# Kernel tuning notes

Hardware: AMD Instinct MI355X
Metric: run time of the kernel (lower is better)

## Reference

```python
import jax, jax.numpy as jnp
import numpy as np
import math

B, CIN, H, W = 8, 64, 128, 128
IC = 128           # inter_channel
CMIN = 32
FN = 3             # feature_num
PLANES = CMIN * 2  # BNL planes
GROUPS = 8
ORDER = 2
GAMMA = 1e-4
FEAT_SHAPES = [(64, 128, 128), (128, 64, 64), (256, 32, 32)]

_pm_cache = {}

def _pool_mat(n, s):
    # adaptive avg-pool matrix [s, n] (torch AdaptiveAvgPool2d bin rule)
    key = (n, s)
    if key not in _pm_cache:
        m = np.zeros((s, n), np.float32)
        for j in range(s):
            a = (j * n) // s
            b = -((-(j + 1) * n) // s)
            m[j, a:b] = 1.0 / (b - a)
        _pm_cache[key] = jnp.asarray(m)
    return _pm_cache[key]

def _pap(x):
    # pyramidAP: adaptive avg pool to 1,3,6,8 and flatten -> [b,c,110]
    b, c, hh, ww = x.shape
    outs = []
    for s in (1, 3, 6, 8):
        ph, pw = _pool_mat(hh, s), _pool_mat(ww, s)
        outs.append(jnp.einsum('ph,bchw,qw->bcpq', ph, x, pw).reshape(b, c, s * s))
    return jnp.concatenate(outs, axis=2)

def _c1x1(w, x):
    return jnp.einsum('oi,bihw->bohw', w, x)

def _pad1(x):
    # kernel_size=1, padding=1 conv == 1x1 conv then zero-pad spatially by 1
    return jnp.pad(x, ((0, 0), (0, 0), (1, 1), (1, 1)))

def _conv3(w, x):
    return jax.lax.conv_general_dilated(x, w, (1, 1), 'SAME',
                                        dimension_numbers=('NCHW', 'OIHW', 'NCHW'))

def _bnl(x_high, x_low, t_w, p_w, g_w, z_w, gn_w, gn_b):
    b, c, h, w = x_high.shape
    # per-group flattened 'single token' vectors of length (planes/G)*h*w
    t = _c1x1(t_w, x_high).reshape(b, GROUPS, -1)
    p = _c1x1(p_w, x_low).reshape(b, GROUPS, -1)
    g = _c1x1(g_w, x_low).reshape(b, GROUPS, -1)
    alphas = [math.sqrt((2 * GAMMA) ** k / math.factorial(k) * math.exp(-2 * GAMMA))
              for k in range(ORDER + 1)]
    t_tay = jnp.stack([t ** k * alphas[k] for k in range(ORDER + 1)], axis=2)  # [b,G,3,N]
    p_tay = jnp.stack([p ** k * alphas[k] for k in range(ORDER + 1)], axis=2)
    att = jnp.einsum('bgkn,bgn->bgk', p_tay, g)          # [b,G,3]
    x = jnp.einsum('bgk,bgkn->bgn', att, t_tay).reshape(b, PLANES, h, w)
    # grouped 1x1 conv z (groups=8)
    x = jnp.einsum('goi,bgihw->bgohw', z_w,
                   x.reshape(b, GROUPS, PLANES // GROUPS, h, w)).reshape(b, c, h, w)
    # GroupNorm(8, 64)
    xg = x.reshape(b, GROUPS, -1)
    mu = xg.mean(-1, keepdims=True)
    var = xg.var(-1, keepdims=True)
    xn = ((xg - mu) / jnp.sqrt(var + 1e-5)).reshape(b, c, h, w)
    xn = xn * gn_w[None, :, None, None] + gn_b[None, :, None, None]
    return xn + x_high

def setup_inputs() -> dict:
    key = jax.random.key(0)
    ks = iter(jax.random.split(key, 64))
    def rn(shape, scale=1.0):
        return jax.random.normal(next(ks), shape, jnp.float32) * scale
    inp = {'input_g': rn((B, CIN, H, W)), 'input_c': rn((B, CIN, H, W))}
    for i, (c, hh, ww) in enumerate(FEAT_SHAPES):
        inp[f'fg_{i}'] = rn((B, c, hh, ww))
        inp[f'fc_{i}'] = rn((B, c, hh, ww))
        for nm in ('k1', 'v1', 'k2', 'v2'):
            inp[f'{nm}_w_{i}'] = rn((IC, c), 0.05)
    inp['q1_w'] = rn((IC, CIN, 3, 3), 0.05)
    inp['q2_w'] = rn((IC, CIN, 3, 3), 0.05)
    inp['mask1_w'] = rn((CIN, IC + CIN), 0.05)
    inp['mask2_w'] = rn((CIN, IC + CIN), 0.05)
    inp['fuse1_w'] = rn((CIN, CIN * FN), 0.05)
    inp['fuse2_w'] = rn((CIN, CIN * FN), 0.05)
    inp['t_w'] = rn((PLANES, CIN), 0.05)
    inp['p_w'] = rn((PLANES, CIN), 0.05)
    inp['g_w'] = rn((PLANES, CIN), 0.05)
    inp['z_w'] = rn((GROUPS, CIN // GROUPS, PLANES // GROUPS), 0.05)
    inp['gn_w'] = jnp.ones((CIN,), jnp.float32)
    inp['gn_b'] = jnp.zeros((CIN,), jnp.float32)
    return inp

def reference(input_g, input_c, fg_0, fg_1, fg_2, fc_0, fc_1, fc_2,
              q1_w, q2_w,
              k1_w_0, v1_w_0, k2_w_0, v2_w_0,
              k1_w_1, v1_w_1, k2_w_1, v2_w_1,
              k1_w_2, v1_w_2, k2_w_2, v2_w_2,
              mask1_w, mask2_w, fuse1_w, fuse2_w,
              t_w, p_w, g_w, z_w, gn_w, gn_b):
    b, c, h, w = input_g.shape
    n = h * w
    x_q1 = _conv3(q1_w, input_g).reshape(b, IC, n)
    x_q2 = _conv3(q2_w, input_c).reshape(b, IC, n)
    fgs = [fg_0, fg_1, fg_2]
    fcs = [fc_0, fc_1, fc_2]
    k1s = [k1_w_0, k1_w_1, k1_w_2]
    v1s = [v1_w_0, v1_w_1, v1_w_2]
    k2s = [k2_w_0, k2_w_1, k2_w_2]
    v2s = [v2_w_0, v2_w_1, v2_w_2]
    grays, colors = [], []
    for i in range(FN):
        xk1 = _pap(_pad1(_c1x1(k1s[i], fcs[i])))   # [b,IC,110]
        xk2 = _pap(_pad1(_c1x1(k2s[i], fgs[i])))
        xv1 = _pap(_pad1(_c1x1(v1s[i], fcs[i])))
        xv2 = _pap(_pad1(_c1x1(v2s[i], fgs[i])))
        kq1 = jax.nn.softmax(jnp.clip(jnp.einsum('bcp,bcn->bpn', xk1, x_q1), -64, 64), axis=1)
        kq2 = jax.nn.softmax(jnp.clip(jnp.einsum('bcp,bcn->bpn', xk2, x_q2), -64, 64), axis=1)
        vkq1 = jnp.einsum('bcp,bpn->bcn', xv1, kq1).reshape(b, IC, h, w)
        vkq2 = jnp.einsum('bcp,bpn->bcn', xv2, kq2).reshape(b, IC, h, w)
        grays.append(_c1x1(mask1_w, jnp.concatenate([input_g, vkq1], 1)))
        colors.append(_c1x1(mask2_w, jnp.concatenate([input_c, vkq2], 1)))
    x_gray = jnp.tanh(_c1x1(fuse1_w, jnp.concatenate(grays, 1))) + input_g
    x_color = jnp.tanh(_c1x1(fuse2_w, jnp.concatenate(colors, 1))) + input_c
    return _bnl(x_gray, x_color, t_w, p_w, g_w, z_w, gn_w, gn_b) + input_g
```

## Files before the change

### kernel.cpp

```cpp
#include <hip/hip_runtime.h>
#include <math.h>

constexpr int    BB      = 8;
constexpr int    NN      = 16384;
constexpr size_t SZ_XQ_ST = (size_t)BB * 128 * NN;
constexpr size_t SZ_XF_ST = (size_t)BB * 64 * NN;

constexpr size_t OFF_XQ   = 0;
constexpr size_t OFF_XT   = 16777216;
constexpr size_t OFF_XF   = 33554432;
constexpr size_t OFF_XG   = OFF_XF + 8388608;
constexpr size_t OFF_POOL = OFF_XF + 2 * SZ_XF_ST;
constexpr size_t OFF_XK   = OFF_POOL + 788480;
constexpr size_t OFF_XV   = OFF_XK + 344064;
constexpr size_t OFF_MT   = OFF_XV + 688128;
constexpr size_t OFF_W    = OFF_MT + 393216;
constexpr size_t OFF_AT   = OFF_W + 73728;
constexpr size_t OFF_WT   = OFF_AT + 4096;
constexpr size_t OFF_ATTC = OFF_WT + 12288;
constexpr size_t OFF_MV   = OFF_ATTC + 192;
constexpr size_t OFF_PART = OFF_MV + 128;
constexpr size_t OFF_PART2= OFF_PART + 98304;

#define A0SQ 0.9998000199986667f
#define A1SQ 1.9996000399973335e-4f
#define A2SQ 1.9996000399973334e-8f

typedef __attribute__((ext_vector_type(8))) short bf16x8;
typedef __attribute__((ext_vector_type(4))) float f32x4;

__device__ inline ushort f2bf(float f) {
    uint u = __float_as_uint(f);
    return (ushort)((u + 0x7fffu + ((u >> 16) & 1u)) >> 16);
}
__device__ inline float bf2f(ushort u) { return __uint_as_float((uint)u << 16); }
__device__ inline uint pk2bf(float lo, float hi) {
    return (uint)f2bf(lo) | ((uint)f2bf(hi) << 16);
}

__global__ __launch_bounds__(256) void k_xt(const float* __restrict__ in0, const float* __restrict__ in1,
                                            ushort* __restrict__ xt0, ushort* __restrict__ xt1) {
    __shared__ float L[64 * 130];
    const int y = blockIdx.x, b = blockIdx.y, tid = threadIdx.x;
    const float* in = blockIdx.z ? in1 : in0;
    ushort* xt = blockIdx.z ? xt1 : xt0;
    const float* ib = in + (((size_t)b * 64) << 14) + (y << 7);
    for (int r = 0; r < 32; ++r) {
        int idx = tid + (r << 8); int ch = idx >> 7; int x = idx & 127;
        L[ch * 130 + x] = ib[((size_t)ch << 14) + x];
    }
    __syncthreads();
    const int x = tid >> 1, seg = tid & 1;
    ushort* ob = xt + ((size_t)(b * 128 + y) * 128 + x) * 64 + seg * 32;
    uint pk[16];
#pragma unroll
    for (int c = 0; c < 16; ++c)
        pk[c] = pk2bf(L[(seg * 32 + 2 * c) * 130 + x], L[(seg * 32 + 2 * c + 1) * 130 + x]);
    uint4* o4 = (uint4*)ob;
#pragma unroll
    for (int c = 0; c < 4; ++c) o4[c] = make_uint4(pk[4 * c], pk[4 * c + 1], pk[4 * c + 2], pk[4 * c + 3]);
}

__global__ __launch_bounds__(256) void k_wt(const float* __restrict__ w1, const float* __restrict__ w2,
                                            ushort* __restrict__ wt1, ushort* __restrict__ wt2) {
    int id = blockIdx.x * 256 + threadIdx.x;
    if (id >= 147456) return;
    int cs = id / 73728; int rem = id - cs * 73728;
    int t = rem >> 13; int oc = (rem >> 6) & 127; int ic = rem & 63;
    const float* w = cs ? w2 : w1;
    (cs ? wt2 : wt1)[rem] = f2bf(w[((size_t)(oc * 64 + ic)) * 9 + t]);
}

__global__ __launch_bounds__(256, 2) void k_convm2(const ushort* __restrict__ Xt0, const ushort* __restrict__ Xt1,
                                                   const ushort* __restrict__ Wt0, const ushort* __restrict__ Wt1,
                                                   ushort* __restrict__ out_base) {
    __shared__ ushort smem[3 * 130 * 72];
    const int tid = threadIdx.x;
    const int y = blockIdx.x, b = blockIdx.y;
    const ushort* Xt = blockIdx.z ? Xt1 : Xt0;
    const ushort* Wt = blockIdx.z ? Wt1 : Wt0;
    ushort* out = out_base + (size_t)blockIdx.z * 16777216;
    const int l = tid & 63;
    const int wv = __builtin_amdgcn_readfirstlane(tid >> 6);
    const int lr = l & 15;
    const int q = l >> 4;

    for (int slot = tid; slot < 390; slot += 256) {
        int dy = slot / 130, xx = slot - dy * 130;
        int row = y + dy - 1, sx = xx - 1;
        bool v = (row >= 0) & (row < 128) & (sx >= 0) & (sx < 128);
        const uint4* s = (const uint4*)(Xt + (((size_t)(b * 128 + row) * 128 + sx) * 64));
        uint4* d = (uint4*)(smem + (size_t)slot * 72);
        uint4 z = make_uint4(0, 0, 0, 0);
#pragma unroll
        for (int j = 0; j < 8; ++j) d[j] = v ? s[j] : z;
    }
    __syncthreads();

    f32x4 acc[2][8];
#pragma unroll
    for (int f = 0; f < 2; ++f)
#pragma unroll
        for (int g = 0; g < 8; ++g)
// ... 7 lines not shown
        for (int h = 0; h < 2; ++h) {
            const int ko = h * 32 + q * 8;
            bf16x8 a0 = *(const bf16x8*)(Wt + ((size_t)(t * 128 + wv * 32 + lr) * 64 + ko));
            bf16x8 a1 = *(const bf16x8*)(Wt + ((size_t)(t * 128 + wv * 32 + 16 + lr) * 64 + ko));
#pragma unroll
            for (int g = 0; g < 8; ++g) {
                bf16x8 bb = *(const bf16x8*)(smem + (size_t)(dy * 130 + g * 16 + lr + dx) * 72 + ko);
                acc[0][g] = __builtin_amdgcn_mfma_f32_16x16x32_bf16(a0, bb, acc[0][g], 0, 0, 0);
                acc[1][g] = __builtin_amdgcn_mfma_f32_16x16x32_bf16(a1, bb, acc[1][g], 0, 0, 0);
            }
        }
    }
    __syncthreads();
    uint* T = (uint*)smem;
#pragma unroll
    for (int f = 0; f < 2; ++f)
#pragma unroll
        for (int g = 0; g < 8; ++g) {
            int dw = (g * 16 + lr) * 68 + wv * 16 + f * 8 + q * 2;
            T[dw] = pk2bf(acc[f][g][0], acc[f][g][1]);
            T[dw + 1] = pk2bf(acc[f][g][2], acc[f][g][3]);
        }
    __syncthreads();
    const int x = tid >> 1, sg = tid & 1;
    ushort* ob = out + ((size_t)(b * 128 + y) * 128 + x) * 128 + sg * 64;
    const uint* src = &T[x * 68 + sg * 32];
#pragma unroll
    for (int j = 0; j < 8; ++j) {
        uint4 vv = *(const uint4*)(src + 4 * j);
        *(uint4*)(ob + j * 8) = vv;
    }
}

struct PoolPtrs { const float* src[6]; };

__global__ __launch_bounds__(256) void k_pool2(PoolPtrs pp, float* __restrict__ ws) {
    extern __shared__ float P[];
    const int blk = blockIdx.x;
    const int tid = threadIdx.x;
    if (blk < 1024) {
        const int tI = (blk < 512) ? 0 : 3;
        const int local = (blk < 512) ? blk : blk - 512;
        const size_t toff = (tI == 0) ? 0 : 394240;
        const int h = 128, stride = 129;
        const float* img = pp.src[tI] + (size_t)local * h * h;
        for (int f = tid; f < h * h; f += 256) {
            int r = f >> 7; int cc = f & 127;
            P[r * stride + cc] = img[f];
        }
        __syncthreads();
        if (tid < h) {
            float cur = 0.f; const int rb = tid * stride;
            for (int cc = 0; cc < h; ++cc) { cur += P[rb + cc]; P[rb + cc] = cur; }
        }
        __syncthreads();
        if (tid < h) {
            float cur = 0.f;
            for (int r = 0; r < h; ++r) { int a = r * stride + tid; cur += P[a]; P[a] = cur; }
        }
        __syncthreads();
        if (tid < 110) {
            int s, off2;
            if (tid == 0)      { s = 1; off2 = 0; }
            else if (tid < 10) { s = 3; off2 = 1; }
            else if (tid < 46) { s = 6; off2 = 10; }
            else               { s = 8; off2 = 46; }
            int r = tid - off2; int j = r / s; int q = r - j * s;
            const int n = h + 2;
            int ra = (j * n) / s,       rb2 = ((j + 1) * n + s - 1) / s;
            int ca = (q * n) / s,       cb2 = ((q + 1) * n + s - 1) / s;
            float area = (float)((rb2 - ra) * (cb2 - ca));
            int r0 = ra - 1; if (r0 < 0) r0 = 0;  int r1 = rb2 - 1; if (r1 > h) r1 = h;
            int c0 = ca - 1; if (c0 < 0) c0 = 0;  int c1 = cb2 - 1; if (c1 > h) c1 = h;
            float ssum = 0.f;
            if (r1 > r0 && c1 > c0) {
                int ri = r1 - 1, rj = r0 - 1, ci = c1 - 1, cj = c0 - 1;
                float f11 = P[ri * stride + ci];
                float f01 = (rj < 0) ? 0.f : P[rj * stride + ci];
                float f10 = (cj < 0) ? 0.f : P[ri * stride + cj];
                float f00 = (rj < 0 || cj < 0) ? 0.f : P[rj * stride + cj];
                ssum = f11 - f01 - f10 + f00;
            }
            ws[OFF_POOL + toff + (size_t)local * 110 + tid] = ssum / area;
        }
    } else {
        int h, hs, tI, local0;
        if (blk < 1536) {
            h = 64; hs = 6;
            if (blk < 1280) { tI = 1; local0 = (blk - 1024) * 4; }
            else            { tI = 4; local0 = (blk - 1280) * 4; }
        } else {
            h = 32; hs = 5;
            if (blk < 1792) { tI = 2; local0 = (blk - 1536) * 8; }
            else            { tI = 5; local0 = (blk - 1792) * 8; }
        }
        const size_t toff = (tI == 1) ? 56320 : (tI == 4) ? 450560 : (tI == 2) ? 168960 : 563200;
        const int lg = tid >> hs;
        const int lr = tid & (h - 1);
        const int stride = h + 1;
        float* Pb = P + (size_t)lg * h * stride;
        const float* img = pp.src[tI] + (size_t)(local0 + lg) * h * h;
        for (int f = lr; f < h * h; f += h) {
            int r = f >> hs; int cc = f & (h - 1);
            Pb[r * stride + cc] = img[f];
        }
        __syncthreads();
        {
            float cur = 0.f; const int rb = lr * stride;
            for (int cc = 0; cc < h; ++cc) { cur += Pb[rb + cc]; Pb[rb + cc] = cur; }
        }
        __syncthreads();
        {
            float cur = 0.f;
            for (int r = 0; r < h; ++r) { int a = r * stride + lr; cur += Pb[a]; Pb[a] = cur; }
        }
        __syncthreads();
        for (int t = lr; t < 110; t += h) {
            int s, off2;
            if (t == 0)      { s = 1; off2 = 0; }
            else if (t < 10) { s = 3; off2 = 1; }
            else if (t < 46) { s = 6; off2 = 10; }
            else             { s = 8; off2 = 46; }
            int r = t - off2; int j = r / s; int q = r - j * s;
            const int n = h + 2;
            int ra = (j * n) / s,       rb2 = ((j + 1) * n + s - 1) / s;
            int ca = (q * n) / s,       cb2 = ((q + 1) * n + s - 1) / s;
            float area = (float)((rb2 - ra) * (cb2 - ca));
            int r0 = ra - 1; if (r0 < 0) r0 = 0;  int r1 = rb2 - 1; if (r1 > h) r1 = h;
            int c0 = ca - 1; if (c0 < 0) c0 = 0;  int c1 = cb2 - 1; if (c1 > h) c1 = h;
            float ssum = 0.f;
            if (r1 > r0 && c1 > c0) {
                int ri = r1 - 1, rj = r0 - 1, ci = c1 - 1, cj = c0 - 1;
                float f11 = Pb[ri * stride + ci];
                float f01 = (rj < 0) ? 0.f : Pb[rj * stride + ci];
                float f10 = (cj < 0) ? 0.f : Pb[ri * stride + cj];
                float f00 = (rj < 0 || cj < 0) ? 0.f : Pb[rj * stride + cj];
                ssum = f11 - f01 - f10 + f00;
            }
            ws[OFF_POOL + toff + (size_t)(local0 + lg) * 110 + t] = ssum / area;
        }
    }
}

__global__ __launch_bounds__(256) void k_pkw(const float* __restrict__ f1, const float* __restrict__ f2,
                                             const float* __restrict__ m1, const float* __restrict__ m2,
                                             const float* __restrict__ tw, const float* __restrict__ pw,
                                             const float* __restrict__ gw, float* __restrict__ ws) {
    int id = blockIdx.x * 256 + threadIdx.x;
    if (id < 73728) {
        int c = id % 192; int t = id / 192; int o = t & 63; int t2 = t >> 6; int i = t2 % 3; int st = t2 / 3;
        const float* fu = st ? f2 : f1; const float* ma = st ? m2 : m1;
        float s = 0.f;
        for (int k = 0; k < 64; ++k) s = fmaf(fu[o * 192 + i * 64 + k], ma[k * 192 + c], s);
        ws[OFF_W + id] = s;
    } else if (id < 81920) {
        int x = id - 73728; int o = x & 63; int c = (x >> 6) & 63; int st = x >> 12;
        const float* fu = st ? f2 : f1; const float* ma = st ? m2 : m1;
        float s = 0.f;
        for (int k = 0; k < 192; ++k) s = fmaf(fu[o * 192 + k], ma[(k & 63) * 192 + c], s);
        ((ushort*)(ws + OFF_AT))[(size_t)st * 4096 + o * 64 + c] = f2bf(s);
    } else if (id < 94208) {
        int x = id - 81920; int c = x & 63; int o = (x >> 6) & 63; int f = x >> 12;
        const float* src = (f == 0) ? tw : ((f == 1) ? pw : gw);
        ((ushort*)(ws + OFF_WT))[(size_t)f * 4096 + o * 64 + c] = f2bf(src[o * 64 + c]);
    }
}

struct KvPtrs { const float* k1[3]; const float* k2[3]; const float* v1[3]; const float* v2[3]; };

__global__ __launch_bounds__(256) void k_xkxv(KvPtrs kp, float* __restrict__ ws) {
    int id = blockIdx.x * 256 + threadIdx.x;
    int isV = 0;
    if (id >= 688128) { isV = 1; id -= 688128; }
    int p = id % 112; int t1 = id / 112; int C = t1 & 127; int t2 = t1 >> 7;
    int b = t2 & 7; int t3 = t2 >> 3; int i = t3 % 3; int st = t3 / 3;
    const int ci = 64 << i;
    size_t poff = (size_t)st * 394240 + (i >= 1 ? 56320 : 0) + (i >= 2 ? 112640 : 0);
    const float* kw = isV ? (st ? kp.v2[i] : kp.v1[i]) : (st ? kp.k2[i] : kp.k1[i]);
    float s = 0.f;
    if (p < 110) {
        const float* pl = ws + OFF_POOL + poff + (size_t)b * ci * 110 + p;
        for (int ic = 0; ic < ci; ++ic) s = fmaf(kw[C * ci + ic], pl[(size_t)ic * 110], s);
    }
    if (isV) ws[OFF_XV + id] = s;
    else     ((ushort*)(ws + OFF_XK))[(size_t)t2 * 14336 + p * 128 + C] = f2bf(s);
}

__global__ __launch_bounds__(256) void k_mt(float* __restrict__ ws) {
    int id = blockIdx.x * 256 + threadIdx.x;
    int p = id & 127; int o = (id >> 7) & 63; int t2 = id >> 13;
    int sti = t2 >> 3;
    float s = 0.f;
    if (p < 110) {
        const float* Wrow = ws + OFF_W + ((size_t)sti * 64 + o) * 192 + 64;
        const float* xv = ws + OFF_XV + (size_t)t2 * 128 * 112 + p;
        for (int r = 0; r < 128; ++r) s = fmaf(Wrow[r], xv[(size_t)r * 112], s);
    }
    ((ushort*)(ws + OFF_MT))[id] = f2bf(s);
}

__global__ __launch_bounds__(256, 2) void k_attn7(float* __restrict__ ws,
                                                  const float* __restrict__ g_in,
                                                  const float* __restrict__ c_in) {
    __shared__ uint pbuf[128 * 68];
    const int tid = threadIdx.x;
    const int w = __builtin_amdgcn_readfirstlane(tid >> 6);
    const int l = tid & 63;
    const int lr = l & 15;
    const int g4 = l >> 4;
    const int n0 = blockIdx.x << 7;
    const int b = blockIdx.y;
    const int st = blockIdx.z;

    const ushort* xqb = (const ushort*)(ws + OFF_XQ);
    const ushort* xkb = (const ushort*)(ws + OFF_XK);
    const ushort* mtb = (const ushort*)(ws + OFF_MT);
    const ushort* atb = (const ushort*)(ws + OFF_AT) + (size_t)st * 4096;
    const ushort* xt  = (const ushort*)(ws + OFF_XT) + (size_t)st * 8388608 + ((size_t)b << 14) * 64;

    {
        int row = w * 32 + (l >> 1);
        int dcol = 56 + ((l & 1) << 2);
#pragma unroll
        for (int j = 0; j < 4; ++j) pbuf[row * 68 + dcol + j] = 0;
    }
    const int ng0 = n0 + (2 * w + 0) * 16 + lr;
    const int ng1 = n0 + (2 * w + 1) * 16 + lr;
    const int row0 = w * 32 + lr;
    const int row1 = w * 32 + 16 + lr;
// ... 206 lines not shown
                    bf16x8 a_p = *(const bf16x8*)(wtb + 4096 + ao);
                    bf16x8 a_g = *(const bf16x8*)(wtb + 8192 + ao);
                    ap_[m] = __builtin_amdgcn_mfma_f32_16x16x32_bf16(a_p, bx, ap_[m], 0, 0, 0);
                    ag_[m] = __builtin_amdgcn_mfma_f32_16x16x32_bf16(a_g, bx, ag_[m], 0, 0, 0);
                }
            }
#pragma unroll
            for (int m = 0; m < 4; ++m)
#pragma unroll
                for (int r = 0; r < 4; ++r) {
                    float pv = ap_[m][r], gv = ag_[m][r];
                    s[m][0] += gv;
                    s[m][1] = fmaf(pv, gv, s[m][1]);
                    s[m][2] = fmaf(pv * pv, gv, s[m][2]);
                }
        }
#pragma unroll
        for (int off = 1; off < 32; off <<= 1)
#pragma unroll
            for (int m = 0; m < 4; ++m)
#pragma unroll
                for (int k = 0; k < 3; ++k) s[m][k] += __shfl_xor(s[m][k], off);
        if (l == 0 || l == 32) {
            const int h = g4 >> 1;
#pragma unroll
            for (int m = 0; m < 4; ++m)
#pragma unroll
                for (int k = 0; k < 3; ++k)
                    ws[OFF_PART + (size_t)((b * 8 + 2 * m + h) * 3 + k) * 512 + blockIdx.x * 4 + w] = s[m][k];
        }
    }
}

__global__ __launch_bounds__(64) void k_attc(float* __restrict__ ws) {
    const int id = blockIdx.x;
    const int l = threadIdx.x;
    const float4* v = (const float4*)(ws + OFF_PART + (size_t)id * 512 + l * 8);
    float4 a = v[0], b2 = v[1];
    float s = a.x + a.y + a.z + a.w + b2.x + b2.y + b2.z + b2.w;
#pragma unroll
    for (int off = 1; off < 64; off <<= 1) s += __shfl_xor(s, off);
    if (l == 0) ws[OFF_ATTC + id] = s;
}

__global__ __launch_bounds__(256) void k_stats2(float* __restrict__ ws, const float* __restrict__ zw) {
    __shared__ float r0[256], r1[256];
    const int nc = blockIdx.x, g = blockIdx.y, b = blockIdx.z, tid = threadIdx.x;
    const ushort* tfb = (const ushort*)(ws + OFF_XF) + ((size_t)(b * 64 + g * 8) << 14);
    const float* a = ws + OFF_ATTC + (size_t)(b * 8 + g) * 3;
    const float c0 = A0SQ * a[0], c1 = A1SQ * a[1], c2 = A2SQ * a[2];
    const float* z = zw + (size_t)g * 64;
    float sum = 0.f, ssq = 0.f;
    for (int n = nc * 2048 + tid; n < (nc + 1) * 2048; n += 256) {
        float y[8];
#pragma unroll
        for (int pl = 0; pl < 8; ++pl) { float tv = bf2f(tfb[((size_t)pl << 14) + n]); y[pl] = fmaf(fmaf(c2, tv, c1), tv, c0); }
#pragma unroll
        for (int o = 0; o < 8; ++o) {
            float xz = 0.f;
#pragma unroll
            for (int i2 = 0; i2 < 8; ++i2) xz = fmaf(z[o * 8 + i2], y[i2], xz);
            sum += xz; ssq = fmaf(xz, xz, ssq);
        }
    }
    r0[tid] = sum; r1[tid] = ssq;
    __syncthreads();
    for (int w = 128; w > 0; w >>= 1) {
        if (tid < w) { r0[tid] += r0[tid + w]; r1[tid] += r1[tid + w]; }
        __syncthreads();
    }
    if (tid == 0) {
        float* p2 = ws + OFF_PART2 + (size_t)((b * 8 + g) * 8 + nc) * 2;
        p2[0] = r0[0]; p2[1] = r1[0];
    }
}

__global__ __launch_bounds__(64) void k_mv(float* __restrict__ ws) {
    const int t = threadIdx.x;
    float sum = 0.f, ssq = 0.f;
    const float* p2 = ws + OFF_PART2 + (size_t)t * 16;
#pragma unroll
    for (int nc = 0; nc < 8; ++nc) { sum += p2[nc * 2]; ssq += p2[nc * 2 + 1]; }
    float mean = sum * (1.f / 131072.f);
    float var = ssq * (1.f / 131072.f) - mean * mean;
    float* mv = ws + OFF_MV + (size_t)t * 2;
    mv[0] = mean; mv[1] = rsqrtf(var + 1e-5f);
}

__global__ __launch_bounds__(256) void k_final(float* __restrict__ ws, const float* __restrict__ zw,
                                               const float* __restrict__ gnw, const float* __restrict__ gnb,
                                               const float* __restrict__ g_in, float* __restrict__ out) {
    int id = blockIdx.x * 256 + threadIdx.x;
    int n = id & 16383; int g = (id >> 14) & 7; int b = id >> 17;
    const float* a = ws + OFF_ATTC + (size_t)(b * 8 + g) * 3;
    const float c0 = A0SQ * a[0], c1 = A1SQ * a[1], c2 = A2SQ * a[2];
    const float* mv = ws + OFF_MV + (size_t)(b * 8 + g) * 2;
    const float mean = mv[0], istd = mv[1];
    const float* z = zw + (size_t)g * 64;
    const ushort* tfb = (const ushort*)(ws + OFF_XF) + ((size_t)(b * 64 + g * 8) << 14) + n;
    float y[8];
#pragma unroll
    for (int pl = 0; pl < 8; ++pl) { float tv = bf2f(tfb[(size_t)pl << 14]); y[pl] = fmaf(fmaf(c2, tv, c1), tv, c0); }
    const ushort* thb = (const ushort*)(ws + OFF_XG) + (((size_t)b << 14) + n) * 64 + g * 8;
    ushort4 u0 = *(const ushort4*)thb;
    ushort4 u1 = *(const ushort4*)(thb + 4);
    float thv[8] = { bf2f(u0.x), bf2f(u0.y), bf2f(u0.z), bf2f(u0.w),
                     bf2f(u1.x), bf2f(u1.y), bf2f(u1.z), bf2f(u1.w) };
    const size_t cb = ((size_t)(b * 64 + g * 8) << 14) + n;
    const float* gi = g_in + cb;
    float* op = out + cb;
#pragma unroll
    for (int o = 0; o < 8; ++o) {
        float xz = 0.f;
#pragma unroll
        for (int i2 = 0; i2 < 8; ++i2) xz = fmaf(z[o * 8 + i2], y[i2], xz);
        int ch = g * 8 + o;
        float base = fmaf((xz - mean) * istd, gnw[ch], gnb[ch]) + thv[o];
        op[(size_t)o << 14] = fmaf(2.f, gi[(size_t)o << 14], base);
    }
}

extern "C" void kernel_launch(void* const* d_in, const int* in_sizes, int n_in,
                              void* d_out, int out_size, void* d_ws, size_t ws_size,
                              hipStream_t stream) {
    const float* in_g = (const float*)d_in[0];
    const float* in_c = (const float*)d_in[1];
    float* ws = (float*)d_ws;
    float* out = (float*)d_out;

    ushort* xqb  = (ushort*)(ws + OFF_XQ);
    ushort* xt_g = (ushort*)(ws + OFF_XT);
    ushort* xt_c = xt_g + 8388608;
    ushort* wt_g = (ushort*)(ws + OFF_XF);
    ushort* wt_c = wt_g + 73728;

    k_xt<<<dim3(128, 8, 2), 256, 0, stream>>>(in_g, in_c, xt_g, xt_c);
    k_wt<<<576, 256, 0, stream>>>((const float*)d_in[20], (const float*)d_in[21], wt_g, wt_c);

    k_convm2<<<dim3(128, 8, 2), 256, 0, stream>>>(xt_g, xt_c, wt_g, wt_c, xqb);

    PoolPtrs pp;
    pp.src[0] = (const float*)d_in[3];  pp.src[1] = (const float*)d_in[9];  pp.src[2] = (const float*)d_in[15];
    pp.src[3] = (const float*)d_in[2];  pp.src[4] = (const float*)d_in[8];  pp.src[5] = (const float*)d_in[14];
    k_pool2<<<2048, 256, 66560, stream>>>(pp, ws);

    k_pkw<<<368, 256, 0, stream>>>((const float*)d_in[24], (const float*)d_in[25],
                                   (const float*)d_in[22], (const float*)d_in[23],
                                   (const float*)d_in[26], (const float*)d_in[27],
                                   (const float*)d_in[28], ws);

    KvPtrs kp;
    kp.k1[0] = (const float*)d_in[4];  kp.k1[1] = (const float*)d_in[10]; kp.k1[2] = (const float*)d_in[16];
    kp.k2[0] = (const float*)d_in[6];  kp.k2[1] = (const float*)d_in[12]; kp.k2[2] = (const float*)d_in[18];
    kp.v1[0] = (const float*)d_in[5];  kp.v1[1] = (const float*)d_in[11]; kp.v1[2] = (const float*)d_in[17];
    kp.v2[0] = (const float*)d_in[7];  kp.v2[1] = (const float*)d_in[13]; kp.v2[2] = (const float*)d_in[19];
    k_xkxv<<<5376, 256, 0, stream>>>(kp, ws);

    k_mt<<<3072, 256, 0, stream>>>(ws);

    k_attn7<<<dim3(128, 8, 2), 256, 0, stream>>>(ws, in_g, in_c);

    k_attc<<<192, 64, 0, stream>>>(ws);

    k_stats2<<<dim3(8, 8, 8), 256, 0, stream>>>(ws, (const float*)d_in[29]);
    k_mv<<<1, 64, 0, stream>>>(ws);
    k_final<<<4096, 256, 0, stream>>>(ws, (const float*)d_in[29], (const float*)d_in[30],
                                      (const float*)d_in[31], in_g, out);
}
```

Baseline: 540.6 us.

## Merge prep kernels, reassociate value-weight product, and fold tiny reductions into neighbors

Folds the transpose, weight conversion, weight-packing and pyramid pooling kernels into one launch. It also reassociates the value path so the fused mask weight is multiplied into the value conv weights first (a small weight-only product) instead of into pooled features per batch. The attention-coefficient and mean/variance reduction kernels are absorbed into the stats and final kernels. The goal is to cut launch count and some per-batch FLOPs. The cost is redundant small reductions per block and a heavier, heterogeneous prep kernel with large shared memory applied to all its blocks.

```diff
diff --git a/kernel.cpp b/kernel.cpp
--- a/kernel.cpp
+++ b/kernel.cpp
@@ -38,37 +38,170 @@
     return (uint)f2bf(lo) | ((uint)f2bf(hi) << 16);
 }
 
-__global__ __launch_bounds__(256) void k_xt(const float* __restrict__ in0, const float* __restrict__ in1,
-                                            ushort* __restrict__ xt0, ushort* __restrict__ xt1) {
-    __shared__ float L[64 * 130];
-    const int y = blockIdx.x, b = blockIdx.y, tid = threadIdx.x;
-    const float* in = blockIdx.z ? in1 : in0;
-    ushort* xt = blockIdx.z ? xt1 : xt0;
-    const float* ib = in + (((size_t)b * 64) << 14) + (y << 7);
-    for (int r = 0; r < 32; ++r) {
-        int idx = tid + (r << 8); int ch = idx >> 7; int x = idx & 127;
-        L[ch * 130 + x] = ib[((size_t)ch << 14) + x];
-    }
-    __syncthreads();
-    const int x = tid >> 1, seg = tid & 1;
-    ushort* ob = xt + ((size_t)(b * 128 + y) * 128 + x) * 64 + seg * 32;
-    uint pk[16];
-#pragma unroll
-    for (int c = 0; c < 16; ++c)
-        pk[c] = pk2bf(L[(seg * 32 + 2 * c) * 130 + x], L[(seg * 32 + 2 * c + 1) * 130 + x]);
-    uint4* o4 = (uint4*)ob;
-#pragma unroll
-    for (int c = 0; c < 4; ++c) o4[c] = make_uint4(pk[4 * c], pk[4 * c + 1], pk[4 * c + 2], pk[4 * c + 3]);
-}
-
-__global__ __launch_bounds__(256) void k_wt(const float* __restrict__ w1, const float* __restrict__ w2,
-                                            ushort* __restrict__ wt1, ushort* __restrict__ wt2) {
-    int id = blockIdx.x * 256 + threadIdx.x;
-    if (id >= 147456) return;
-    int cs = id / 73728; int rem = id - cs * 73728;
-    int t = rem >> 13; int oc = (rem >> 6) & 127; int ic = rem & 63;
-    const float* w = cs ? w2 : w1;
-    (cs ? wt2 : wt1)[rem] = f2bf(w[((size_t)(oc * 64 + ic)) * 9 + t]);
+struct PrepPtrs {
+    const float* in_g; const float* in_c;
+    const float* w1;  const float* w2;
+    const float* f1;  const float* f2; const float* m1; const float* m2;
+    const float* tw;  const float* pw; const float* gw;
+    const float* pool[6];
+};
+
+__global__ __launch_bounds__(256) void k_prep(PrepPtrs pp, float* __restrict__ ws) {
+    extern __shared__ float P[];
+    const int blk = blockIdx.x;
+    const int tid = threadIdx.x;
+    if (blk < 2048) {
+        const int z = blk >> 10, b = (blk >> 7) & 7, y = blk & 127;
+        const float* in = z ? pp.in_c : pp.in_g;
+        ushort* xt = (ushort*)(ws + OFF_XT) + (size_t)z * 8388608;
+        float* L = P;
+        const float* ib = in + (((size_t)b * 64) << 14) + (y << 7);
+        for (int r = 0; r < 32; ++r) {
+            int idx = tid + (r << 8); int ch = idx >> 7; int x = idx & 127;
+            L[ch * 130 + x] = ib[((size_t)ch << 14) + x];
+        }
+        __syncthreads();
+        const int x = tid >> 1, seg = tid & 1;
+        ushort* ob = xt + ((size_t)(b * 128 + y) * 128 + x) * 64 + seg * 32;
+        uint pk[16];
+#pragma unroll
+        for (int c = 0; c < 16; ++c)
+            pk[c] = pk2bf(L[(seg * 32 + 2 * c) * 130 + x], L[(seg * 32 + 2 * c + 1) * 130 + x]);
+        uint4* o4 = (uint4*)ob;
+#pragma unroll
+        for (int c = 0; c < 4; ++c) o4[c] = make_uint4(pk[4 * c], pk[4 * c + 1], pk[4 * c + 2], pk[4 * c + 3]);
+    } else if (blk < 2624) {
+        int id = (blk - 2048) * 256 + tid;
+        if (id >= 147456) return;
+        int cs = id / 73728; int rem = id - cs * 73728;
+        int t = rem >> 13; int oc = (rem >> 6) & 127; int ic = rem & 63;
+        const float* w = cs ? pp.w2 : pp.w1;
+        ushort* wt = (ushort*)(ws + OFF_XF) + (size_t)cs * 73728;
+        wt[rem] = f2bf(w[((size_t)(oc * 64 + ic)) * 9 + t]);
+    } else if (blk < 2992) {
+        int id = (blk - 2624) * 256 + tid;
+        if (id < 73728) {
+            int c = id % 192; int t = id / 192; int o = t & 63; int t2 = t >> 6; int i = t2 % 3; int st = t2 / 3;
+            const float* fu = st ? pp.f2 : pp.f1; const float* ma = st ? pp.m2 : pp.m1;
+            float s = 0.f;
+            for (int k = 0; k < 64; ++k) s = fmaf(fu[o * 192 + i * 64 + k], ma[k * 192 + c], s);
+            ws[OFF_W + id] = s;
+        } else if (id < 81920) {
+            int x = id - 73728; int o = x & 63; int c = (x >> 6) & 63; int st = x >> 12;
+            const float* fu = st ? pp.f2 : pp.f1; const float* ma = st ? pp.m2 : pp.m1;
+            float s = 0.f;
+            for (int k = 0; k < 192; ++k) s = fmaf(fu[o * 192 + k], ma[(k & 63) * 192 + c], s);
+            ((ushort*)(ws + OFF_AT))[(size_t)st * 4096 + o * 64 + c] = f2bf(s);
+        } else if (id < 94208) {
+            int x = id - 81920; int c = x & 63; int o = (x >> 6) & 63; int f = x >> 12;
+            const float* src = (f == 0) ? pp.tw : ((f == 1) ? pp.pw : pp.gw);
+            ((ushort*)(ws + OFF_WT))[(size_t)f * 4096 + o * 64 + c] = f2bf(src[o * 64 + c]);
+        }
+    } else {
+        const int pblk = blk - 2992;
+        if (pblk < 1024) {
+            const int tI = (pblk < 512) ? 0 : 3;
+            const int local = (pblk < 512) ? pblk : pblk - 512;
+            const size_t toff = (tI == 0) ? 0 : 394240;
+            const int h = 128, stride = 129;
+            const float* img = pp.pool[tI] + (size_t)local * h * h;
+            for (int f = tid; f < h * h; f += 256) {
+                int r = f >> 7; int cc = f & 127;
+                P[r * stride + cc] = img[f];
+            }
+            __syncthreads();
+            if (tid < h) {
+                float cur = 0.f; const int rb = tid * stride;
+                for (int cc = 0; cc < h; ++cc) { cur += P[rb + cc]; P[rb + cc] = cur; }
+            }
+            __syncthreads();
+            if (tid < h) {
+                float cur = 0.f;
+                for (int r = 0; r < h; ++r) { int a = r * stride + tid; cur += P[a]; P[a] = cur; }
+            }
+            __syncthreads();
+            if (tid < 110) {
+                int s, off2;
+                if (tid == 0)      { s = 1; off2 = 0; }
+                else if (tid < 10) { s = 3; off2 = 1; }
+                else if (tid < 46) { s = 6; off2 = 10; }
+                else               { s = 8; off2 = 46; }
+                int r = tid - off2; int j = r / s; int q = r - j * s;
+                const int n = h + 2;
+                int ra = (j * n) / s,       rb2 = ((j + 1) * n + s - 1) / s;
+                int ca = (q * n) / s,       cb2 = ((q + 1) * n + s - 1) / s;
+                float area = (float)((rb2 - ra) * (cb2 - ca));
+                int r0 = ra - 1; if (r0 < 0) r0 = 0;  int r1 = rb2 - 1; if (r1 > h) r1 = h;
+                int c0 = ca - 1; if (c0 < 0) c0 = 0;  int c1 = cb2 - 1; if (c1 > h) c1 = h;
+                float ssum = 0.f;
+                if (r1 > r0 && c1 > c0) {
+                    int ri = r1 - 1, rj = r0 - 1, ci = c1 - 1, cj = c0 - 1;
+                    float f11 = P[ri * stride + ci];
+                    float f01 = (rj < 0) ? 0.f : P[rj * stride + ci];
+                    float f10 = (cj < 0) ? 0.f : P[ri * stride + cj];
+                    float f00 = (rj < 0 || cj < 0) ? 0.f : P[rj * stride + cj];
+                    ssum = f11 - f01 - f10 + f00;
+                }
+                ws[OFF_POOL + toff + (size_t)local * 110 + tid] = ssum / area;
+            }
+        } else {
+            int h, hs, tI, local0;
+            if (pblk < 1536) {
+                h = 64; hs = 6;
+                if (pblk < 1280) { tI = 1; local0 = (pblk - 1024) * 4; }
+                else             { tI = 4; local0 = (pblk - 1280) * 4; }
+            } else {
+                h = 32; hs = 5;
+                if (pblk < 1792) { tI = 2; local0 = (pblk - 1536) * 8; }
+                else             { tI = 5; local0 = (pblk - 1792) * 8; }
+            }
+            const size_t toff = (tI == 1) ? 56320 : (tI == 4) ? 450560 : (tI == 2) ? 168960 : 563200;
+            const int lg = tid >> hs;
+            const int lr = tid & (h - 1);
+            const int stride = h + 1;
+            float* Pb = P + (size_t)lg * h * stride;
+            const float* img = pp.pool[tI] + (size_t)(local0 + lg) * h * h;
+            for (int f = lr; f < h * h; f += h) {
+                int r = f >> hs; int cc = f & (h - 1);
+                Pb[r * stride + cc] = img[f];
+            }
+            __syncthreads();
+            {
+                float cur = 0.f; const int rb = lr * stride;
+                for (int cc = 0; cc < h; ++cc) { cur += Pb[rb + cc]; Pb[rb + cc] = cur; }
+            }
+            __syncthreads();
+            {
+                float cur = 0.f;
+                for (int r = 0; r < h; ++r) { int a = r * stride + lr; cur += Pb[a]; Pb[a] = cur; }
+            }
+            __syncthreads();
+            for (int t = lr; t < 110; t += h) {
+                int s, off2;
+                if (t == 0)      { s = 1; off2 = 0; }
+                else if (t < 10) { s = 3; off2 = 1; }
+                else if (t < 46) { s = 6; off2 = 10; }
+                else             { s = 8; off2 = 46; }
+                int r = t - off2; int j = r / s; int q = r - j * s;
+                const int n = h + 2;
+                int ra = (j * n) / s,       rb2 = ((j + 1) * n + s - 1) / s;
+                int ca = (q * n) / s,       cb2 = ((q + 1) * n + s - 1) / s;
+                float area = (float)((rb2 - ra) * (cb2 - ca));
+                int r0 = ra - 1; if (r0 < 0) r0 = 0;  int r1 = rb2 - 1; if (r1 > h) r1 = h;
+                int c0 = ca - 1; if (c0 < 0) c0 = 0;  int c1 = cb2 - 1; if (c1 > h) c1 = h;
+                float ssum = 0.f;
+                if (r1 > r0 && c1 > c0) {
+                    int ri = r1 - 1, rj = r0 - 1, ci = c1 - 1, cj = c0 - 1;
+                    float f11 = Pb[ri * stride + ci];
+                    float f01 = (rj < 0) ? 0.f : Pb[rj * stride + ci];
+                    float f10 = (cj < 0) ? 0.f : Pb[ri * stride + cj];
+                    float f00 = (rj < 0 || cj < 0) ? 0.f : Pb[rj * stride + cj];
+                    ssum = f11 - f01 - f10 + f00;
+                }
+                ws[OFF_POOL + toff + (size_t)(local0 + lg) * 110 + t] = ssum / area;
+            }
+        }
+    }
 }
 
 __global__ __launch_bounds__(256, 2) void k_convm2(const ushort* __restrict__ Xt0, const ushort* __restrict__ Xt1,
@@ -142,169 +275,50 @@
     }
 }
 
-struct PoolPtrs { const float* src[6]; };
-
-__global__ __launch_bounds__(256) void k_pool2(PoolPtrs pp, float* __restrict__ ws) {
-    extern __shared__ float P[];
-    const int blk = blockIdx.x;
-    const int tid = threadIdx.x;
-    if (blk < 1024) {
-        const int tI = (blk < 512) ? 0 : 3;
-        const int local = (blk < 512) ? blk : blk - 512;
-        const size_t toff = (tI == 0) ? 0 : 394240;
-        const int h = 128, stride = 129;
-        const float* img = pp.src[tI] + (size_t)local * h * h;
-        for (int f = tid; f < h * h; f += 256) {
-            int r = f >> 7; int cc = f & 127;
-            P[r * stride + cc] = img[f];
-        }
-        __syncthreads();
-        if (tid < h) {
-            float cur = 0.f; const int rb = tid * stride;
-            for (int cc = 0; cc < h; ++cc) { cur += P[rb + cc]; P[rb + cc] = cur; }
-        }
-        __syncthreads();
-        if (tid < h) {
-            float cur = 0.f;
-            for (int r = 0; r < h; ++r) { int a = r * stride + tid; cur += P[a]; P[a] = cur; }
-        }
-        __syncthreads();
-        if (tid < 110) {
-            int s, off2;
-            if (tid == 0)      { s = 1; off2 = 0; }
-            else if (tid < 10) { s = 3; off2 = 1; }
-            else if (tid < 46) { s = 6; off2 = 10; }
-            else               { s = 8; off2 = 46; }
-            int r = tid - off2; int j = r / s; int q = r - j * s;
-            const int n = h + 2;
-            int ra = (j * n) / s,       rb2 = ((j + 1) * n + s - 1) / s;
-            int ca = (q * n) / s,       cb2 = ((q + 1) * n + s - 1) / s;
-            float area = (float)((rb2 - ra) * (cb2 - ca));
-            int r0 = ra - 1; if (r0 < 0) r0 = 0;  int r1 = rb2 - 1; if (r1 > h) r1 = h;
-            int c0 = ca - 1; if (c0 < 0) c0 = 0;  int c1 = cb2 - 1; if (c1 > h) c1 = h;
-            float ssum = 0.f;
-            if (r1 > r0 && c1 > c0) {
-                int ri = r1 - 1, rj = r0 - 1, ci = c1 - 1, cj = c0 - 1;
-                float f11 = P[ri * stride + ci];
-                float f01 = (rj < 0) ? 0.f : P[rj * stride + ci];
-                float f10 = (cj < 0) ? 0.f : P[ri * stride + cj];
-                float f00 = (rj < 0 || cj < 0) ? 0.f : P[rj * stride + cj];
-                ssum = f11 - f01 - f10 + f00;
-            }
-            ws[OFF_POOL + toff + (size_t)local * 110 + tid] = ssum / area;
-        }
+struct KvPtrs { const float* k1[3]; const float* k2[3]; const float* v1[3]; const float* v2[3]; };
+
+__global__ __launch_bounds__(256) void k_xkwv(KvPtrs kp, float* __restrict__ ws) {
+    int id = blockIdx.x * 256 + threadIdx.x;
+    if (id < 688128) {
+        int p = id % 112; int t1 = id / 112; int C = t1 & 127; int t2 = t1 >> 7;
+        int b = t2 & 7; int t3 = t2 >> 3; int i = t3 % 3; int st = t3 / 3;
+        const int ci = 64 << i;
+        size_t poff = (size_t)st * 394240 + (i >= 1 ? 56320 : 0) + (i >= 2 ? 112640 : 0);
+        const float* kw = st ? kp.k2[i] : kp.k1[i];
+        float s = 0.f;
+        if (p < 110) {
+            const float* pl = ws + OFF_POOL + poff + (size_t)b * ci * 110 + p;
+            for (int ic = 0; ic < ci; ++ic) s = fmaf(kw[C * ci + ic], pl[(size_t)ic * 110], s);
+        }
+        ((ushort*)(ws + OFF_XK))[(size_t)t2 * 14336 + p * 128 + C] = f2bf(s);
     } else {
-        int h, hs, tI, local0;
-        if (blk < 1536) {
-            h = 64; hs = 6;
-            if (blk < 1280) { tI = 1; local0 = (blk - 1024) * 4; }
-            else            { tI = 4; local0 = (blk - 1280) * 4; }
-        } else {
-            h = 32; hs = 5;
-            if (blk < 1792) { tI = 2; local0 = (blk - 1536) * 8; }
-            else            { tI = 5; local0 = (blk - 1792) * 8; }
-        }
-        const size_t toff = (tI == 1) ? 56320 : (tI == 4) ? 450560 : (tI == 2) ? 168960 : 563200;
-        const int lg = tid >> hs;
-        const int lr = tid & (h - 1);
-        const int stride = h + 1;
-        float* Pb = P + (size_t)lg * h * stride;
-        const float* img = pp.src[tI] + (size_t)(local0 + lg) * h * h;
-        for (int f = lr; f < h * h; f += h) {
-            int r = f >> hs; int cc = f & (h - 1);
-            Pb[r * stride + cc] = img[f];
-        }
-        __syncthreads();
-        {
-            float cur = 0.f; const int rb = lr * stride;
-            for (int cc = 0; cc < h; ++cc) { cur += Pb[rb + cc]; Pb[rb + cc] = cur; }
-        }
-        __syncthreads();
-        {
-            float cur = 0.f;
-            for (int r = 0; r < h; ++r) { int a = r * stride + lr; cur += Pb[a]; Pb[a] = cur; }
-        }
-        __syncthreads();
-        for (int t = lr; t < 110; t += h) {
-            int s, off2;
-            if (t == 0)      { s = 1; off2 = 0; }
-            else if (t < 10) { s = 3; off2 = 1; }
-            else if (t < 46) { s = 6; off2 = 10; }
-            else             { s = 8; off2 = 46; }
-            int r = t - off2; int j = r / s; int q = r - j * s;
-            const int n = h + 2;
-            int ra = (j * n) / s,       rb2 = ((j + 1) * n + s - 1) / s;
-            int ca = (q * n) / s,       cb2 = ((q + 1) * n + s - 1) / s;
-            float area = (float)((rb2 - ra) * (cb2 - ca));
-            int r0 = ra - 1; if (r0 < 0) r0 = 0;  int r1 = rb2 - 1; if (r1 > h) r1 = h;
-            int c0 = ca - 1; if (c0 < 0) c0 = 0;  int c1 = cb2 - 1; if (c1 > h) c1 = h;
-            float ssum = 0.f;
-            if (r1 > r0 && c1 > c0) {
-                int ri = r1 - 1, rj = r0 - 1, ci = c1 - 1, cj = c0 - 1;
-                float f11 = Pb[ri * stride + ci];
-                float f01 = (rj < 0) ? 0.f : Pb[rj * stride + ci];
-                float f10 = (cj < 0) ? 0.f : Pb[ri * stride + cj];
-                float f00 = (rj < 0 || cj < 0) ? 0.f : Pb[rj * stride + cj];
-                ssum = f11 - f01 - f10 + f00;
-            }
-            ws[OFF_POOL + toff + (size_t)(local0 + lg) * 110 + t] = ssum / area;
-        }
-    }
-}
-
-__global__ __launch_bounds__(256) void k_pkw(const float* __restrict__ f1, const float* __restrict__ f2,
-                                             const float* __restrict__ m1, const float* __restrict__ m2,
-                                             const float* __restrict__ tw, const float* __restrict__ pw,
-                                             const float* __restrict__ gw, float* __restrict__ ws) {
+        int x = id - 688128;
+        if (x >= 57344) return;
+        int st = x / 28672; int x2 = x - st * 28672;
+        int i, ci, base;
+        if (x2 < 4096)       { i = 0; ci = 64;  base = 0; }
+        else if (x2 < 12288) { i = 1; ci = 128; base = 4096; }
+        else                 { i = 2; ci = 256; base = 12288; }
+        int rem = x2 - base; int o = rem / ci; int ic = rem - o * ci;
+        const float* vw = st ? kp.v2[i] : kp.v1[i];
+        const float* Wrow = ws + OFF_W + ((size_t)((st * 3 + i) * 64 + o)) * 192 + 64;
+        float s = 0.f;
+        for (int r = 0; r < 128; ++r) s = fmaf(Wrow[r], vw[(size_t)r * ci + ic], s);
+        ws[OFF_XV + (size_t)st * 28672 + x2] = s;
+    }
+}
+
+__global__ __launch_bounds__(256) void k_mt2(float* __restrict__ ws) {
     int id = blockIdx.x * 256 + threadIdx.x;
-    if (id < 73728) {
-        int c = id % 192; int t = id / 192; int o = t & 63; int t2 = t >> 6; int i = t2 % 3; int st = t2 / 3;
-        const float* fu = st ? f2 : f1; const float* ma = st ? m2 : m1;
-        float s = 0.f;
-        for (int k = 0; k < 64; ++k) s = fmaf(fu[o * 192 + i * 64 + k], ma[k * 192 + c], s);
-        ws[OFF_W + id] = s;
-    } else if (id < 81920) {
-        int x = id - 73728; int o = x & 63; int c = (x >> 6) & 63; int st = x >> 12;
-        const float* fu = st ? f2 : f1; const float* ma = st ? m2 : m1;
-        float s = 0.f;
-        for (int k = 0; k < 192; ++k) s = fmaf(fu[o * 192 + k], ma[(k & 63) * 192 + c], s);
-        ((ushort*)(ws + OFF_AT))[(size_t)st * 4096 + o * 64 + c] = f2bf(s);
-    } else if (id < 94208) {
-        int x = id - 81920; int c = x & 63; int o = (x >> 6) & 63; int f = x >> 12;
-        const float* src = (f == 0) ? tw : ((f == 1) ? pw : gw);
-        ((ushort*)(ws + OFF_WT))[(size_t)f * 4096 + o * 64 + c] = f2bf(src[o * 64 + c]);
-    }
-}
-
-struct KvPtrs { const float* k1[3]; const float* k2[3]; const float* v1[3]; const float* v2[3]; };
-
-__global__ __launch_bounds__(256) void k_xkxv(KvPtrs kp, float* __restrict__ ws) {
-    int id = blockIdx.x * 256 + threadIdx.x;
-    int isV = 0;
-    if (id >= 688128) { isV = 1; id -= 688128; }
-    int p = id % 112; int t1 = id / 112; int C = t1 & 127; int t2 = t1 >> 7;
-    int b = t2 & 7; int t3 = t2 >> 3; int i = t3 % 3; int st = t3 / 3;
+    int p = id & 127; int o = (id >> 7) & 63; int t2 = id >> 13;
+    int sti = t2 >> 3; int b = t2 & 7; int i = sti % 3; int st = sti / 3;
     const int ci = 64 << i;
-    size_t poff = (size_t)st * 394240 + (i >= 1 ? 56320 : 0) + (i >= 2 ? 112640 : 0);
-    const float* kw = isV ? (st ? kp.v2[i] : kp.v1[i]) : (st ? kp.k2[i] : kp.k1[i]);
     float s = 0.f;
     if (p < 110) {
+        size_t poff = (size_t)st * 394240 + (i >= 1 ? 56320 : 0) + (i >= 2 ? 112640 : 0);
         const float* pl = ws + OFF_POOL + poff + (size_t)b * ci * 110 + p;
-        for (int ic = 0; ic < ci; ++ic) s = fmaf(kw[C * ci + ic], pl[(size_t)ic * 110], s);
-    }
-    if (isV) ws[OFF_XV + id] = s;
-    else     ((ushort*)(ws + OFF_XK))[(size_t)t2 * 14336 + p * 128 + C] = f2bf(s);
-}
-
-__global__ __launch_bounds__(256) void k_mt(float* __restrict__ ws) {
-    int id = blockIdx.x * 256 + threadIdx.x;
-    int p = id & 127; int o = (id >> 7) & 63; int t2 = id >> 13;
-    int sti = t2 >> 3;
-    float s = 0.f;
-    if (p < 110) {
-        const float* Wrow = ws + OFF_W + ((size_t)sti * 64 + o) * 192 + 64;
-        const float* xv = ws + OFF_XV + (size_t)t2 * 128 * 112 + p;
-        for (int r = 0; r < 128; ++r) s = fmaf(Wrow[r], xv[(size_t)r * 112], s);
+        const float* wv = ws + OFF_XV + (size_t)st * 28672 + (i >= 1 ? 4096 : 0) + (i >= 2 ? 8192 : 0) + o * ci;
+        for (int ic = 0; ic < ci; ++ic) s = fmaf(wv[ic], pl[(size_t)ic * 110], s);
     }
     ((ushort*)(ws + OFF_MT))[id] = f2bf(s);
 }
@@ -577,23 +591,27 @@
     }
 }
 
-__global__ __launch_bounds__(64) void k_attc(float* __restrict__ ws) {
-    const int id = blockIdx.x;
-    const int l = threadIdx.x;
-    const float4* v = (const float4*)(ws + OFF_PART + (size_t)id * 512 + l * 8);
-    float4 a = v[0], b2 = v[1];
-    float s = a.x + a.y + a.z + a.w + b2.x + b2.y + b2.z + b2.w;
-#pragma unroll
-    for (int off = 1; off < 64; off <<= 1) s += __shfl_xor(s, off);
-    if (l == 0) ws[OFF_ATTC + id] = s;
-}
-
-__global__ __launch_bounds__(256) void k_stats2(float* __restrict__ ws, const float* __restrict__ zw) {
+__global__ __launch_bounds__(256) void k_stats3(float* __restrict__ ws, const float* __restrict__ zw) {
     __shared__ float r0[256], r1[256];
+    __shared__ float ac3[3];
     const int nc = blockIdx.x, g = blockIdx.y, b = blockIdx.z, tid = threadIdx.x;
+    {
+        int k = tid >> 6; int lane = tid & 63;
+        if (k < 3) {
+            const float* v = ws + OFF_PART + (size_t)((b * 8 + g) * 3 + k) * 512;
+            float s = 0.f;
+            for (int j = lane; j < 512; j += 64) s += v[j];
+#pragma unroll
+            for (int off = 1; off < 64; off <<= 1) s += __shfl_xor(s, off);
+            if (lane == 0) {
+                ac3[k] = s;
+                if (nc == 0) ws[OFF_ATTC + (size_t)(b * 8 + g) * 3 + k] = s;
+            }
+        }
+        __syncthreads();
+    }
+    const float c0 = A0SQ * ac3[0], c1 = A1SQ * ac3[1], c2 = A2SQ * ac3[2];
     const ushort* tfb = (const ushort*)(ws + OFF_XF) + ((size_t)(b * 64 + g * 8) << 14);
-    const float* a = ws + OFF_ATTC + (size_t)(b * 8 + g) * 3;
-    const float c0 = A0SQ * a[0], c1 = A1SQ * a[1], c2 = A2SQ * a[2];
     const float* z = zw + (size_t)g * 64;
     float sum = 0.f, ssq = 0.f;
     for (int n = nc * 2048 + tid; n < (nc + 1) * 2048; n += 256) {
@@ -620,27 +638,22 @@
     }
 }
 
-__global__ __launch_bounds__(64) void k_mv(float* __restrict__ ws) {
-    const int t = threadIdx.x;
-    float sum = 0.f, ssq = 0.f;
-    const float* p2 = ws + OFF_PART2 + (size_t)t * 16;
-#pragma unroll
-    for (int nc = 0; nc < 8; ++nc) { sum += p2[nc * 2]; ssq += p2[nc * 2 + 1]; }
-    float mean = sum * (1.f / 131072.f);
-    float var = ssq * (1.f / 131072.f) - mean * mean;
-    float* mv = ws + OFF_MV + (size_t)t * 2;
-    mv[0] = mean; mv[1] = rsqrtf(var + 1e-5f);
-}
-
-__global__ __launch_bounds__(256) void k_final(float* __restrict__ ws, const float* __restrict__ zw,
-                                               const float* __restrict__ gnw, const float* __restrict__ gnb,
-                                               const float* __restrict__ g_in, float* __restrict__ out) {
+__global__ __launch_bounds__(256) void k_final2(float* __restrict__ ws, const float* __restrict__ zw,
+                                                const float* __restrict__ gnw, const float* __restrict__ gnb,
+                                                const float* __restrict__ g_in, float* __restrict__ out) {
     int id = blockIdx.x * 256 + threadIdx.x;
     int n = id & 16383; int g = (id >> 14) & 7; int b = id >> 17;
     const float* a = ws + OFF_ATTC + (size_t)(b * 8 + g) * 3;
     const float c0 = A0SQ * a[0], c1 = A1SQ * a[1], c2 = A2SQ * a[2];
-    const float* mv = ws + OFF_MV + (size_t)(b * 8 + g) * 2;
-    const float mean = mv[0], istd = mv[1];
+    float sum = 0.f, ssq = 0.f;
+    {
+        const float* p2 = ws + OFF_PART2 + (size_t)(b * 8 + g) * 16;
+#pragma unroll
+        for (int ncc = 0; ncc < 8; ++ncc) { sum += p2[ncc * 2]; ssq += p2[ncc * 2 + 1]; }
+    }
+    const float mean = sum * (1.f / 131072.f);
+    const float var = ssq * (1.f / 131072.f) - mean * mean;
+    const float istd = rsqrtf(var + 1e-5f);
     const float* z = zw + (size_t)g * 64;
     const ushort* tfb = (const ushort*)(ws + OFF_XF) + ((size_t)(b * 64 + g * 8) << 14) + n;
     float y[8];
@@ -679,36 +692,30 @@
     ushort* wt_g = (ushort*)(ws + OFF_XF);
     ushort* wt_c = wt_g + 73728;
 
-    k_xt<<<dim3(128, 8, 2), 256, 0, stream>>>(in_g, in_c, xt_g, xt_c);
-    k_wt<<<576, 256, 0, stream>>>((const float*)d_in[20], (const float*)d_in[21], wt_g, wt_c);
+    PrepPtrs pp;
+    pp.in_g = in_g; pp.in_c = in_c;
+    pp.w1 = (const float*)d_in[20]; pp.w2 = (const float*)d_in[21];
+    pp.f1 = (const float*)d_in[24]; pp.f2 = (const float*)d_in[25];
+    pp.m1 = (const float*)d_in[22]; pp.m2 = (const float*)d_in[23];
+    pp.tw = (const float*)d_in[26]; pp.pw = (const float*)d_in[27]; pp.gw = (const float*)d_in[28];
+    pp.pool[0] = (const float*)d_in[3];  pp.pool[1] = (const float*)d_in[9];  pp.pool[2] = (const float*)d_in[15];
+    pp.pool[3] = (const float*)d_in[2];  pp.pool[4] = (const float*)d_in[8];  pp.pool[5] = (const float*)d_in[14];
+    k_prep<<<5040, 256, 66560, stream>>>(pp, ws);
 
     k_convm2<<<dim3(128, 8, 2), 256, 0, stream>>>(xt_g, xt_c, wt_g, wt_c, xqb);
-
-    PoolPtrs pp;
-    pp.src[0] = (const float*)d_in[3];  pp.src[1] = (const float*)d_in[9];  pp.src[2] = (const float*)d_in[15];
-    pp.src[3] = (const float*)d_in[2];  pp.src[4] = (const float*)d_in[8];  pp.src[5] = (const float*)d_in[14];
-    k_pool2<<<2048, 256, 66560, stream>>>(pp, ws);
-
-    k_pkw<<<368, 256, 0, stream>>>((const float*)d_in[24], (const float*)d_in[25],
-                                   (const float*)d_in[22], (const float*)d_in[23],
-                                   (const float*)d_in[26], (const float*)d_in[27],
-                                   (const float*)d_in[28], ws);
 
     KvPtrs kp;
     kp.k1[0] = (const float*)d_in[4];  kp.k1[1] = (const float*)d_in[10]; kp.k1[2] = (const float*)d_in[16];
     kp.k2[0] = (const float*)d_in[6];  kp.k2[1] = (const float*)d_in[12]; kp.k2[2] = (const float*)d_in[18];
     kp.v1[0] = (const float*)d_in[5];  kp.v1[1] = (const float*)d_in[11]; kp.v1[2] = (const float*)d_in[17];
     kp.v2[0] = (const float*)d_in[7];  kp.v2[1] = (const float*)d_in[13]; kp.v2[2] = (const float*)d_in[19];
-    k_xkxv<<<5376, 256, 0, stream>>>(kp, ws);
-
-    k_mt<<<3072, 256, 0, stream>>>(ws);
+    k_xkwv<<<2912, 256, 0, stream>>>(kp, ws);
+
+    k_mt2<<<3072, 256, 0, stream>>>(ws);
 
     k_attn7<<<dim3(128, 8, 2), 256, 0, stream>>>(ws, in_g, in_c);
 
-    k_attc<<<192, 64, 0, stream>>>(ws);
-
-    k_stats2<<<dim3(8, 8, 8), 256, 0, stream>>>(ws, (const float*)d_in[29]);
-    k_mv<<<1, 64, 0, stream>>>(ws);
-    k_final<<<4096, 256, 0, stream>>>(ws, (const float*)d_in[29], (const float*)d_in[30],
-                                      (const float*)d_in[31], in_g, out);
-}
+    k_stats3<<<dim3(8, 8, 8), 256, 0, stream>>>(ws, (const float*)d_in[29]);
+    k_final2<<<4096, 256, 0, stream>>>(ws, (const float*)d_in[29], (const float*)d_in[30],
+                                       (const float*)d_in[31], in_g, out);
+}
```

Result: slower. 591.0 us (+9.3%).

## Fold mask weights into value weights before applying to pooled features

Applied to the files above, without the earlier changes.

The old path projected the pooled features through the value weights (128 outputs) and then multiplied by the folded mask/fuse weights. The new path first multiplies the mask weights by the value-conv weights to form a small 64×ci matrix, then applies that to the pooled features directly. This cuts the per-batch value projection work and the intermediate XV buffer, and roughly halves the grid of the first kernel. Because it reassociates the matrix products, floating-point rounding changes slightly.

```diff
diff --git a/kernel.cpp b/kernel.cpp
--- a/kernel.cpp
+++ b/kernel.cpp
@@ -278,33 +278,48 @@
 
 struct KvPtrs { const float* k1[3]; const float* k2[3]; const float* v1[3]; const float* v2[3]; };
 
-__global__ __launch_bounds__(256) void k_xkxv(KvPtrs kp, float* __restrict__ ws) {
+__global__ __launch_bounds__(256) void k_xkwv(KvPtrs kp, float* __restrict__ ws) {
     int id = blockIdx.x * 256 + threadIdx.x;
-    int isV = 0;
-    if (id >= 688128) { isV = 1; id -= 688128; }
-    int p = id % 112; int t1 = id / 112; int C = t1 & 127; int t2 = t1 >> 7;
-    int b = t2 & 7; int t3 = t2 >> 3; int i = t3 % 3; int st = t3 / 3;
+    if (id < 688128) {
+        int p = id % 112; int t1 = id / 112; int C = t1 & 127; int t2 = t1 >> 7;
+        int b = t2 & 7; int t3 = t2 >> 3; int i = t3 % 3; int st = t3 / 3;
+        const int ci = 64 << i;
+        size_t poff = (size_t)st * 394240 + (i >= 1 ? 56320 : 0) + (i >= 2 ? 112640 : 0);
+        const float* kw = st ? kp.k2[i] : kp.k1[i];
+        float s = 0.f;
+        if (p < 110) {
+            const float* pl = ws + OFF_POOL + poff + (size_t)b * ci * 110 + p;
+            for (int ic = 0; ic < ci; ++ic) s = fmaf(kw[C * ci + ic], pl[(size_t)ic * 110], s);
+        }
+        ((ushort*)(ws + OFF_XK))[(size_t)t2 * 14336 + p * 128 + C] = f2bf(s);
+    } else {
+        int x = id - 688128;
+        if (x >= 57344) return;
+        int st = x / 28672; int x2 = x - st * 28672;
+        int i, ci, base;
+        if (x2 < 4096)       { i = 0; ci = 64;  base = 0; }
+        else if (x2 < 12288) { i = 1; ci = 128; base = 4096; }
+        else                 { i = 2; ci = 256; base = 12288; }
+        int rem = x2 - base; int o = rem / ci; int ic = rem - o * ci;
+        const float* vw = st ? kp.v2[i] : kp.v1[i];
+        const float* Wrow = ws + OFF_W + ((size_t)((st * 3 + i) * 64 + o)) * 192 + 64;
+        float s = 0.f;
+        for (int r = 0; r < 128; ++r) s = fmaf(Wrow[r], vw[(size_t)r * ci + ic], s);
+        ws[OFF_XV + (size_t)st * 28672 + x2] = s;
+    }
+}
+
+__global__ __launch_bounds__(256) void k_mt2(float* __restrict__ ws) {
+    int id = blockIdx.x * 256 + threadIdx.x;
+    int p = id & 127; int o = (id >> 7) & 63; int t2 = id >> 13;
+    int sti = t2 >> 3; int b = t2 & 7; int i = sti % 3; int st = sti / 3;
     const int ci = 64 << i;
-    size_t poff = (size_t)st * 394240 + (i >= 1 ? 56320 : 0) + (i >= 2 ? 112640 : 0);
-    const float* kw = isV ? (st ? kp.v2[i] : kp.v1[i]) : (st ? kp.k2[i] : kp.k1[i]);
     float s = 0.f;
     if (p < 110) {
+        size_t poff = (size_t)st * 394240 + (i >= 1 ? 56320 : 0) + (i >= 2 ? 112640 : 0);
         const float* pl = ws + OFF_POOL + poff + (size_t)b * ci * 110 + p;
-        for (int ic = 0; ic < ci; ++ic) s = fmaf(kw[C * ci + ic], pl[(size_t)ic * 110], s);
-    }
-    if (isV) ws[OFF_XV + id] = s;
-    else     ((ushort*)(ws + OFF_XK))[(size_t)t2 * 14336 + p * 128 + C] = f2bf(s);
-}
-
-__global__ __launch_bounds__(256) void k_mt(float* __restrict__ ws) {
-    int id = blockIdx.x * 256 + threadIdx.x;
-    int p = id & 127; int o = (id >> 7) & 63; int t2 = id >> 13;
-    int sti = t2 >> 3;
-    float s = 0.f;
-    if (p < 110) {
-        const float* Wrow = ws + OFF_W + ((size_t)sti * 64 + o) * 192 + 64;
-        const float* xv = ws + OFF_XV + (size_t)t2 * 128 * 112 + p;
-        for (int r = 0; r < 128; ++r) s = fmaf(Wrow[r], xv[(size_t)r * 112], s);
+        const float* wv = ws + OFF_XV + (size_t)st * 28672 + (i >= 1 ? 4096 : 0) + (i >= 2 ? 8192 : 0) + o * ci;
+        for (int ic = 0; ic < ci; ++ic) s = fmaf(wv[ic], pl[(size_t)ic * 110], s);
     }
     ((ushort*)(ws + OFF_MT))[id] = f2bf(s);
 }
@@ -699,9 +714,9 @@
     kp.k2[0] = (const float*)d_in[6];  kp.k2[1] = (const float*)d_in[12]; kp.k2[2] = (const float*)d_in[18];
     kp.v1[0] = (const float*)d_in[5];  kp.v1[1] = (const float*)d_in[11]; kp.v1[2] = (const float*)d_in[17];
     kp.v2[0] = (const float*)d_in[7];  kp.v2[1] = (const float*)d_in[13]; kp.v2[2] = (const float*)d_in[19];
-    k_xkxv<<<5376, 256, 0, stream>>>(kp, ws);
-
-    k_mt<<<3072, 256, 0, stream>>>(ws);
+    k_xkwv<<<2912, 256, 0, stream>>>(kp, ws);
+
+    k_mt2<<<3072, 256, 0, stream>>>(ws);
 
     k_attn7<<<dim3(128, 8, 2), 256, 0, stream>>>(ws, in_g, in_c);
 
```

After: 606.7 us. 12.2% more time.
